# Kernel tuning notes

Measured on AMD Instinct MI355X. Metric: run time of the kernel, lower is better.

The kernel has to match this reference:

```python
import jax, jax.numpy as jnp
import numpy as np

N_NODES = 50000


def _gcn_norm(edge_index, n):
    # add self loops, compute symmetric normalization coefficients
    src = jnp.concatenate([edge_index[0], jnp.arange(n, dtype=edge_index.dtype)])
    dst = jnp.concatenate([edge_index[1], jnp.arange(n, dtype=edge_index.dtype)])
    deg = jax.ops.segment_sum(jnp.ones_like(dst, dtype=jnp.float32), dst, num_segments=n)
    dis = jnp.where(deg > 0, jax.lax.rsqrt(jnp.maximum(deg, 1.0)), 0.0)
    norm = dis[src] * dis[dst]  # [E+n]
    return src, dst, norm


def _gcn_conv(x, W, b, src, dst, norm, n):
    xw = x @ W                      # [n, out]
    msg = xw[src] * norm[:, None]   # gather + scale
    out = jax.ops.segment_sum(msg, dst, num_segments=n)
    return out + b


def setup_inputs() -> dict:
    key = jax.random.key(0)
    ks = jax.random.split(key, 12)
    n, d, h, E, P = N_NODES, 512, 512, 400000, 200000
    sc = lambda fan_in: 1.0 / np.sqrt(fan_in)
    return {
        "x": jax.random.normal(ks[0], (n, d), dtype=jnp.float32),
        "edge_index": jax.random.randint(ks[1], (2, E), 0, n, dtype=jnp.int32),
        "edge_pairs": jax.random.randint(ks[2], (2, P), 0, n, dtype=jnp.int32),
        "W1": jax.random.uniform(ks[3], (d, h), jnp.float32, -sc(d), sc(d)),
        "b1": jnp.zeros((h,), jnp.float32),
        "W2": jax.random.uniform(ks[4], (h, h), jnp.float32, -sc(h), sc(h)),
        "b2": jnp.zeros((h,), jnp.float32),
        "lpW1": jax.random.uniform(ks[5], (2 * h, h), jnp.float32, -sc(2 * h), sc(2 * h)),
        "lpb1": jax.random.uniform(ks[6], (h,), jnp.float32, -sc(2 * h), sc(2 * h)),
        "lpW2": jax.random.uniform(ks[7], (h, 1), jnp.float32, -sc(h), sc(h)),
        "lpb2": jax.random.uniform(ks[8], (1,), jnp.float32, -sc(h), sc(h)),
    }


def reference(x, edge_index, edge_pairs, W1, b1, W2, b2, lpW1, lpb1, lpW2, lpb2):
    n = x.shape[0]
    src, dst, norm = _gcn_norm(edge_index, n)
    # encoder: GCNConv -> relu -> (dropout is identity at inference) -> GCNConv
    z = _gcn_conv(x, W1, b1, src, dst, norm, n)
    z = jax.nn.relu(z)
    z = _gcn_conv(z, W2, b2, src, dst, norm, n)
    # link predictor: gather-concat MLP
    h = jnp.concatenate([z[edge_pairs[0]], z[edge_pairs[1]]], axis=-1)  # [P, 2h]
    h = jax.nn.relu(h @ lpW1 + lpb1)
    logits = (h @ lpW2 + lpb2)[:, 0]
    return jax.nn.sigmoid(logits)
```

## Files before the change

kernel.cpp:

```cpp
#include <hip/hip_runtime.h>
#include <hip/hip_bf16.h>
#include <math.h>

#define TPB 256

typedef __attribute__((ext_vector_type(8))) short bf16x8;
typedef __attribute__((ext_vector_type(4))) float f32x4;

__device__ __forceinline__ unsigned cvt_bf(float f) {
    unsigned u = __float_as_uint(f);
    u += 0x7fffu + ((u >> 16) & 1u);
    return u >> 16;
}
__device__ __forceinline__ unsigned pack2f(float a, float b) {
    __hip_bfloat162 h = __float22bfloat162_rn(float2{a, b});
    unsigned u;
    __builtin_memcpy(&u, &h, 4);
    return u;
}

__device__ __forceinline__ void gload16(const void* g, void* l) {
    __builtin_amdgcn_global_load_lds(
        (const __attribute__((address_space(1))) void*)g,
        (__attribute__((address_space(3))) void*)l, 16, 0, 0);
}


__global__ void k_hist(const int* __restrict__ dst, int* __restrict__ cnt, int E) {
    int e = blockIdx.x * TPB + threadIdx.x;
    if (e < E) atomicAdd(&cnt[dst[e]], 1);
}

__global__ __launch_bounds__(256)
void k_scan1(const int* __restrict__ cnt, int* __restrict__ incl,
             int* __restrict__ bsum, int n) {
    __shared__ int sh[256];
    const int t = threadIdx.x;
    const int i = blockIdx.x * 256 + t;
    int v = (i < n) ? cnt[i] : 0;
    sh[t] = v;
    __syncthreads();
#pragma unroll
    for (int d = 1; d < 256; d <<= 1) {
        int u = (t >= d) ? sh[t - d] : 0;
        __syncthreads();
        sh[t] += u;
        __syncthreads();
    }
    if (i < n) incl[i] = sh[t];
    if (t == 255) bsum[blockIdx.x] = sh[255];
}

__global__ __launch_bounds__(256)
void k_scan2(int* __restrict__ bsum, int* __restrict__ boff,
             int* __restrict__ row_start, int n, int nb) {
    __shared__ int sh[256];
    const int t = threadIdx.x;
    int v = (t < nb) ? bsum[t] : 0;
    sh[t] = v;
    __syncthreads();
#pragma unroll
    for (int d = 1; d < 256; d <<= 1) {
        int u = (t >= d) ? sh[t - d] : 0;
        __syncthreads();
        sh[t] += u;
        __syncthreads();
    }
    if (t < nb) boff[t] = sh[t] - v;
    if (t == nb - 1) row_start[n] = sh[t];
}

__global__ void k_scan3(const int* __restrict__ cnt, const int* __restrict__ incl,
                        const int* __restrict__ boff, int* __restrict__ row_start,
                        int* __restrict__ cursor, float* __restrict__ dis, int n) {
    int i = blockIdx.x * TPB + threadIdx.x;
    if (i >= n) return;
    int c = cnt[i];
    int ex = boff[i >> 8] + incl[i] - c;
    row_start[i] = ex;
    cursor[i] = ex;
    dis[i] = rsqrtf((float)c + 1.0f);
}

__global__ void k_fill_csr(const int* __restrict__ src, const int* __restrict__ dst,
                           const float* __restrict__ dis, int* __restrict__ cursor,
                           int* __restrict__ csr_src, float* __restrict__ csr_nrm, int E) {
    int e = blockIdx.x * TPB + threadIdx.x;
    if (e >= E) return;
    int s = src[e], d = dst[e];
    int pos = atomicAdd(&cursor[d], 1);
    csr_src[pos] = s;
    csr_nrm[pos] = dis[s] * dis[d];
}


__global__ __launch_bounds__(256)
void k_prep(const float* __restrict__ x, unsigned short* __restrict__ xbf, int n8, int nbA,
            const float* __restrict__ W1, unsigned short* __restrict__ w1t,
            const float* __restrict__ W2, unsigned short* __restrict__ w2bf,
            const float* __restrict__ lpW1, unsigned short* __restrict__ lpw1t,
            const float* __restrict__ b2, const float* __restrict__ lpb1,
            float* __restrict__ bias_big) {
    int b = blockIdx.x;
    if (b < nbA) {
        int i = b * TPB + threadIdx.x;
        if (i >= n8) return;
        float4 f0 = *(const float4*)(x + (size_t)i * 8);
        float4 f1 = *(const float4*)(x + (size_t)i * 8 + 4);
        uint4 o;
        o.x = pack2f(f0.x, f0.y); o.y = pack2f(f0.z, f0.w);
        o.z = pack2f(f1.x, f1.y); o.w = pack2f(f1.z, f1.w);
        *(uint4*)(xbf + (size_t)i * 8) = o;
        return;
    }
    b -= nbA;
    if (b < 1024) {
        int id = b * TPB + threadIdx.x;
        int nn = id >> 9, k = id & 511;
        w1t[id] = (unsigned short)cvt_bf(W1[(size_t)k * 512 + nn]);
        return;
    }
    b -= 1024;
    if (b < 128) {
        int i = b * TPB + threadIdx.x;
        float4 f0 = *(const float4*)(W2 + (size_t)i * 8);
        float4 f1 = *(const float4*)(W2 + (size_t)i * 8 + 4);
        uint4 o;
        o.x = pack2f(f0.x, f0.y); o.y = pack2f(f0.z, f0.w);
        o.z = pack2f(f1.x, f1.y); o.w = pack2f(f1.z, f1.w);
        *(uint4*)(w2bf + (size_t)i * 8) = o;
        return;
    }
    b -= 128;
    if (b < 2048) {
        int id = b * TPB + threadIdx.x;
        int j = id >> 9, k = id & 511;
        float v = (j < 512) ? lpW1[(size_t)k * 512 + j]
                            : lpW1[(size_t)(512 + k) * 512 + (j - 512)];
        lpw1t[id] = (unsigned short)cvt_bf(v);
        return;
    }
    b -= 2048;
    {
        const int j = b * 4 + (threadIdx.x >> 6);
        if (j >= 1024) return;
        const int lane = threadIdx.x & 63;
        const int col = (j < 512) ? j : (j - 512);
        const int ro = (j < 512) ? 0 : 512;
        float s = 0.f;
#pragma unroll
        for (int it = 0; it < 8; ++it) {
            int k = lane + it * 64;
            s = fmaf(b2[k], lpW1[(size_t)(ro + k) * 512 + col], s);
        }
        s += __shfl_xor(s, 1, 64);
        s += __shfl_xor(s, 2, 64);
        s += __shfl_xor(s, 4, 64);
        s += __shfl_xor(s, 8, 64);
        s += __shfl_xor(s, 16, 64);
        s += __shfl_xor(s, 32, 64);
        if (lane == 0) bias_big[j] = s + ((j < 512) ? lpb1[j] : 0.f);
    }
}


__device__ __forceinline__ void fma8(float* acc, uint4 u, float r) {
    acc[0] = fmaf(__uint_as_float(u.x << 16), r, acc[0]);
    acc[1] = fmaf(__uint_as_float(u.x & 0xffff0000u), r, acc[1]);
    acc[2] = fmaf(__uint_as_float(u.y << 16), r, acc[2]);
    acc[3] = fmaf(__uint_as_float(u.y & 0xffff0000u), r, acc[3]);
    acc[4] = fmaf(__uint_as_float(u.z << 16), r, acc[4]);
    acc[5] = fmaf(__uint_as_float(u.z & 0xffff0000u), r, acc[5]);
    acc[6] = fmaf(__uint_as_float(u.w << 16), r, acc[6]);
    acc[7] = fmaf(__uint_as_float(u.w & 0xffff0000u), r, acc[7]);
}

__global__ __launch_bounds__(256)
void k_agg_bf(const unsigned short* __restrict__ xin, const int* __restrict__ row_start,
              const int* __restrict__ csr_src, const float* __restrict__ csr_nrm,
              const float* __restrict__ dis, unsigned short* __restrict__ out, int n) {
    const int v = (blockIdx.x * TPB + threadIdx.x) >> 6;
    if (v >= n) return;
    const int lane = threadIdx.x & 63;
    const uint4* base = (const uint4*)xin;

    float d = dis[v]; float d2 = d * d;
    float acc[8];
    {
        uint4 u = base[(size_t)v * 64 + lane];
        acc[0] = d2 * __uint_as_float(u.x << 16);
        acc[1] = d2 * __uint_as_float(u.x & 0xffff0000u);
        acc[2] = d2 * __uint_as_float(u.y << 16);
        acc[3] = d2 * __uint_as_float(u.y & 0xffff0000u);
        acc[4] = d2 * __uint_as_float(u.z << 16);
        acc[5] = d2 * __uint_as_float(u.z & 0xffff0000u);
        acc[6] = d2 * __uint_as_float(u.w << 16);
        acc[7] = d2 * __uint_as_float(u.w & 0xffff0000u);
    }
    const int beg = row_start[v], end = row_start[v + 1];
    int j = beg;
    for (; j + 3 < end; j += 4) {
        int s0 = csr_src[j], s1 = csr_src[j + 1];
        int s2 = csr_src[j + 2], s3 = csr_src[j + 3];
        float r0 = csr_nrm[j], r1 = csr_nrm[j + 1];
        float r2 = csr_nrm[j + 2], r3 = csr_nrm[j + 3];
        uint4 u0 = base[(size_t)s0 * 64 + lane];
        uint4 u1 = base[(size_t)s1 * 64 + lane];
        uint4 u2 = base[(size_t)s2 * 64 + lane];
        uint4 u3 = base[(size_t)s3 * 64 + lane];
        fma8(acc, u0, r0);
        fma8(acc, u1, r1);
        fma8(acc, u2, r2);
        fma8(acc, u3, r3);
    }
    for (; j < end; ++j) {
        uint4 u = base[(size_t)csr_src[j] * 64 + lane];
        fma8(acc, u, csr_nrm[j]);
    }
    uint4 o;
    o.x = pack2f(acc[0], acc[1]); o.y = pack2f(acc[2], acc[3]);
    o.z = pack2f(acc[4], acc[5]); o.w = pack2f(acc[6], acc[7]);
    ((uint4*)out)[(size_t)v * 64 + lane] = o;
}


__global__ __launch_bounds__(256)
void k_gemm_bf(const unsigned short* __restrict__ A, const unsigned short* __restrict__ Bt,
               const float* __restrict__ bias, unsigned short* __restrict__ C,
               int M, int K, int N, int do_relu, int nbx, int m_off, int m_end) {
    const int lin = blockIdx.x;
    const int xcd = lin & 7, seq = lin >> 3;
    const int rowt = xcd + 8 * (seq / nbx);
    const int colt = seq % nbx;
    const int m0 = m_off + rowt * 128;
    if (m0 >= m_end) return;
    const int n0 = colt * 128;

    __shared__ __align__(16) char smem[16384];
    char* Asl = smem;
    char* Bsl = smem + 8192;
    const int t = threadIdx.x;
    const int wid = t >> 6, l = t & 63;
    const int wr = (wid >> 1) * 64, wc = (wid & 1) * 64;
    const int lrow = l & 15, g = l >> 4;

    const int srow = (l >> 2);
    const int cb_src = ((l & 3) * 16) ^ ((srow & 3) << 4);
    const int r0 = wid * 32 + srow, r1 = r0 + 16;
    const size_t rowA0 = (size_t)min(m0 + r0, M - 1) * K * 2;
    const size_t rowA1 = (size_t)min(m0 + r1, M - 1) * K * 2;
    const size_t rowB0 = (size_t)(n0 + r0) * K * 2;
    const size_t rowB1 = (size_t)(n0 + r1) * K * 2;
    const char* Ab = (const char*)A;
    const char* Bb = (const char*)Bt;
    char* ldsA0 = Asl + (wid * 32) * 64;
    char* ldsA1 = ldsA0 + 16 * 64;
    char* ldsB0 = Bsl + (wid * 32) * 64;
    char* ldsB1 = ldsB0 + 16 * 64;
    const int rd_off = (g * 16) ^ ((lrow & 3) << 4);

    f32x4 acc[4][4] = {};
    for (int k0 = 0; k0 < K; k0 += 32) {
        const size_t koff = (size_t)k0 * 2 + cb_src;
        gload16(Ab + rowA0 + koff, ldsA0);
        gload16(Ab + rowA1 + koff, ldsA1);
        gload16(Bb + rowB0 + koff, ldsB0);
        gload16(Bb + rowB1 + koff, ldsB1);
        __syncthreads();
        bf16x8 af[4], bfr[4];
#pragma unroll
        for (int i = 0; i < 4; ++i)
            af[i] = *(const bf16x8*)(Asl + (wr + i * 16 + lrow) * 64 + rd_off);
#pragma unroll
        for (int j = 0; j < 4; ++j)
            bfr[j] = *(const bf16x8*)(Bsl + (wc + j * 16 + lrow) * 64 + rd_off);
#pragma unroll
        for (int i = 0; i < 4; ++i)
#pragma unroll
            for (int j = 0; j < 4; ++j)
                acc[i][j] = __builtin_amdgcn_mfma_f32_16x16x32_bf16(af[i], bfr[j], acc[i][j], 0, 0, 0);
        __syncthreads();
    }

    float bv[4];
#pragma unroll
    for (int j = 0; j < 4; ++j) bv[j] = bias[n0 + wc + j * 16 + lrow];
    float* lws = (float*)(smem + wid * 4096);
    const int rrow = l >> 2, rcol = (l & 3) * 16;
#pragma unroll
    for (int i = 0; i < 4; ++i) {
#pragma unroll
        for (int e = 0; e < 4; ++e)
#pragma unroll
            for (int j = 0; j < 4; ++j) {
                float vv = acc[i][j][e] + bv[j];
                if (do_relu) vv = fmaxf(vv, 0.f);
                lws[(g * 4 + e) * 64 + j * 16 + lrow] = vv;
            }
        asm volatile("s_waitcnt lgkmcnt(0)" ::: "memory");
        __builtin_amdgcn_sched_barrier(0);
        const int grow = m0 + wr + i * 16 + rrow;
        float4 f0 = *(const float4*)&lws[rrow * 64 + rcol];
        float4 f1 = *(const float4*)&lws[rrow * 64 + rcol + 4];
        float4 f2 = *(const float4*)&lws[rrow * 64 + rcol + 8];
        float4 f3 = *(const float4*)&lws[rrow * 64 + rcol + 12];
        if (grow < M) {
            uint4 o0, o1;
            o0.x = pack2f(f0.x, f0.y); o0.y = pack2f(f0.z, f0.w);
            o0.z = pack2f(f1.x, f1.y); o0.w = pack2f(f1.z, f1.w);
            o1.x = pack2f(f2.x, f2.y); o1.y = pack2f(f2.z, f2.w);
            o1.z = pack2f(f3.x, f3.y); o1.w = pack2f(f3.z, f3.w);
            *(uint4*)(C + (size_t)grow * N + n0 + wc + rcol)     = o0;
            *(uint4*)(C + (size_t)grow * N + n0 + wc + rcol + 8) = o1;
        }
        asm volatile("s_waitcnt lgkmcnt(0)" ::: "memory");
        __builtin_amdgcn_sched_barrier(0);
    }
}


__global__ __launch_bounds__(256)
void k_pair(const unsigned short* __restrict__ uv, const int* __restrict__ pair, int P,
            const float* __restrict__ w2, const float* __restrict__ lpb2,
            float* __restrict__ out) {
    const int idx = (blockIdx.x * TPB + threadIdx.x) >> 6;
    if (idx >= P) return;
    const int lane = threadIdx.x & 63;
    const int p0n = pair[idx], p1n = pair[P + idx];
    const uint4 a = *(const uint4*)(uv + (size_t)p0n * 1024 + lane * 8);
    const uint4 b = *(const uint4*)(uv + (size_t)p1n * 1024 + 512 + lane * 8);
    const float4 w0 = *(const float4*)(w2 + lane * 8);
    const float4 w1 = *(const float4*)(w2 + lane * 8 + 4);
    const unsigned ua[4] = {a.x, a.y, a.z, a.w};
    const unsigned ub[4] = {b.x, b.y, b.z, b.w};
    const float wv[8] = {w0.x, w0.y, w0.z, w0.w, w1.x, w1.y, w1.z, w1.w};
    float s = 0.f;
#pragma unroll
    for (int q = 0; q < 4; ++q) {
        float h0 = __uint_as_float(ua[q] << 16) + __uint_as_float(ub[q] << 16);
        float h1 = __uint_as_float(ua[q] & 0xffff0000u) + __uint_as_float(ub[q] & 0xffff0000u);
        s = fmaf(fmaxf(h0, 0.f), wv[2 * q], s);
        s = fmaf(fmaxf(h1, 0.f), wv[2 * q + 1], s);
    }
    s += __shfl_xor(s, 1, 64);
    s += __shfl_xor(s, 2, 64);
    s += __shfl_xor(s, 4, 64);
    s += __shfl_xor(s, 8, 64);
    s += __shfl_xor(s, 16, 64);
    s += __shfl_xor(s, 32, 64);
    if (lane == 0) out[idx] = 1.0f / (1.0f + expf(-(s + lpb2[0])));
}


extern "C" void kernel_launch(void* const* d_in, const int* in_sizes, int n_in,
                              void* d_out, int out_size, void* d_ws, size_t ws_size,
                              hipStream_t stream) {
    const float* x    = (const float*)d_in[0];
    const int*   ei   = (const int*)d_in[1];
    const int*   ep   = (const int*)d_in[2];
    const float* W1   = (const float*)d_in[3];
    const float* b1   = (const float*)d_in[4];
    const float* W2   = (const float*)d_in[5];
    const float* b2   = (const float*)d_in[6];
    const float* lpW1 = (const float*)d_in[7];
    const float* lpb1 = (const float*)d_in[8];
    const float* lpW2 = (const float*)d_in[9];
    const float* lpb2 = (const float*)d_in[10];

    const int n = in_sizes[0] / 512;
    const int E = in_sizes[1] / 2;
    const int P = in_sizes[2] / 2;
    const int* src = ei;
    const int* dst = ei + E;

    char* w = (char*)d_ws;
    size_t off = 0;
    auto alloc = [&](size_t bytes) {
        void* p = w + off;
        off = (off + bytes + 255) & ~(size_t)255;
        return p;
    };
    int*   cnt       = (int*)alloc((size_t)n * 4);
    int*   incl      = (int*)alloc((size_t)n * 4);
    int*   bsum      = (int*)alloc((size_t)256 * 4);
    int*   boff      = (int*)alloc((size_t)256 * 4);
    int*   row_start = (int*)alloc((size_t)(n + 1) * 4);
    int*   cursor    = (int*)alloc((size_t)n * 4);
    int*   csr_src   = (int*)alloc((size_t)E * 4);
    float* csr_nrm   = (float*)alloc((size_t)E * 4);
    float* dis       = (float*)alloc((size_t)n * 4);
    unsigned short* w1t    = (unsigned short*)alloc((size_t)512 * 512 * 2);
    unsigned short* w2bf   = (unsigned short*)alloc((size_t)512 * 512 * 2);
    unsigned short* lpw1t  = (unsigned short*)alloc((size_t)1024 * 512 * 2);
    unsigned short* wfT    = (unsigned short*)alloc((size_t)1024 * 512 * 2);
    float* bias_big  = (float*)alloc((size_t)1024 * 4);
    float* zerob     = (float*)alloc((size_t)1024 * 4);
    unsigned short* bufA = (unsigned short*)alloc((size_t)n * 512 * 2);
    unsigned short* bufB = (unsigned short*)alloc((size_t)n * 512 * 2);
    unsigned short* uv   = (unsigned short*)alloc((size_t)n * 1024 * 2);

    dim3 blk(TPB);
    const int nb_n = (n + TPB - 1) / TPB;
    const int nb_E = (E + TPB - 1) / TPB;
    const int nb_scan = (n + 255) / 256;

    (void)hipMemsetAsync(cnt, 0, (size_t)n * 4, stream);
    (void)hipMemsetAsync(zerob, 0, (size_t)1024 * 4, stream);
    k_hist<<<nb_E, blk, 0, stream>>>(dst, cnt, E);
    k_scan1<<<nb_scan, 256, 0, stream>>>(cnt, incl, bsum, n);
    k_scan2<<<1, 256, 0, stream>>>(bsum, boff, row_start, n, nb_scan);
    k_scan3<<<nb_n, blk, 0, stream>>>(cnt, incl, boff, row_start, cursor, dis, n);
    k_fill_csr<<<nb_E, blk, 0, stream>>>(src, dst, dis, cursor, csr_src, csr_nrm, E);

    const int n8  = n * 64;
    const int nbA = (n8 + TPB - 1) / TPB;
    const int prep_blocks = nbA + 1024 + 128 + 2048 + 256;
    k_prep<<<prep_blocks, blk, 0, stream>>>(x, bufA, n8, nbA, W1, w1t, W2, w2bf,
                                            lpW1, lpw1t, b2, lpb1, bias_big);

    const int gy  = (n + 127) / 128;
    const int gy8 = ((gy + 7) / 8) * 8;
    const int agg_blocks = (n * 64 + TPB - 1) / TPB;

    k_gemm_bf<<<4 * 8, blk, 0, stream>>>(lpw1t, w2bf, zerob, wfT, 1024, 512, 512, 0, 4, 0, 1024);

    k_agg_bf<<<agg_blocks, blk, 0, stream>>>(bufA, row_start, csr_src, csr_nrm, dis, bufB, n);
    k_gemm_bf<<<4 * gy8, blk, 0, stream>>>(bufB, w1t, b1, bufA, n, 512, 512, 1, 4, 0, n);
    k_agg_bf<<<agg_blocks, blk, 0, stream>>>(bufA, row_start, csr_src, csr_nrm, dis, bufB, n);
    {
        const int t1 = (gy + 1) / 2;
        const int g1 = ((t1 + 7) / 8) * 8;
        const int t2 = gy - t1;
        const int g2 = ((t2 + 7) / 8) * 8;
        const int m_split = t1 * 128;
        k_gemm_bf<<<8 * g1, blk, 0, stream>>>(bufB, wfT, bias_big, uv, n, 512, 1024, 0, 8, 0, m_split);
        k_gemm_bf<<<8 * g2, blk, 0, stream>>>(bufB, wfT, bias_big, uv, n, 512, 1024, 0, 8, m_split, n);
    }

    k_pair<<<(P * 64 + TPB - 1) / TPB, blk, 0, stream>>>(uv, ep, P, lpW2, lpb2, (float*)d_out);
}
```

Before: 442.0 us.

## Software-pipeline neighbor gathers in aggregation and merge split final GEMM launch

The aggregation kernel now double-buffers its edge gathers, issuing the next four neighbor-row loads before doing the FMAs on the previous four, so more memory requests stay in flight. Separately, the final encoder-to-predictor GEMM, which was split into two launches over row ranges, becomes a single launch, and the m_off/m_end parameters are removed. The prefetching raises register pressure, and merging the launches removes whatever overlap or cache benefit the split may have offered.

```diff
diff --git a/kernel.cpp b/kernel.cpp
--- a/kernel.cpp
+++ b/kernel.cpp
@@ -199,19 +199,29 @@
     }
     const int beg = row_start[v], end = row_start[v + 1];
     int j = beg;
-    for (; j + 3 < end; j += 4) {
-        int s0 = csr_src[j], s1 = csr_src[j + 1];
-        int s2 = csr_src[j + 2], s3 = csr_src[j + 3];
-        float r0 = csr_nrm[j], r1 = csr_nrm[j + 1];
-        float r2 = csr_nrm[j + 2], r3 = csr_nrm[j + 3];
-        uint4 u0 = base[(size_t)s0 * 64 + lane];
-        uint4 u1 = base[(size_t)s1 * 64 + lane];
-        uint4 u2 = base[(size_t)s2 * 64 + lane];
-        uint4 u3 = base[(size_t)s3 * 64 + lane];
-        fma8(acc, u0, r0);
-        fma8(acc, u1, r1);
-        fma8(acc, u2, r2);
-        fma8(acc, u3, r3);
+    if (end - beg >= 4) {
+        float r[4];
+        uint4 ub[4];
+#pragma unroll
+        for (int q = 0; q < 4; ++q) r[q] = csr_nrm[j + q];
+#pragma unroll
+        for (int q = 0; q < 4; ++q) ub[q] = base[(size_t)csr_src[j + q] * 64 + lane];
+        j += 4;
+        while (j + 3 < end) {
+            float r2[4];
+            uint4 ub2[4];
+#pragma unroll
+            for (int q = 0; q < 4; ++q) r2[q] = csr_nrm[j + q];
+#pragma unroll
+            for (int q = 0; q < 4; ++q) ub2[q] = base[(size_t)csr_src[j + q] * 64 + lane];
+#pragma unroll
+            for (int q = 0; q < 4; ++q) fma8(acc, ub[q], r[q]);
+#pragma unroll
+            for (int q = 0; q < 4; ++q) { ub[q] = ub2[q]; r[q] = r2[q]; }
+            j += 4;
+        }
+#pragma unroll
+        for (int q = 0; q < 4; ++q) fma8(acc, ub[q], r[q]);
     }
     for (; j < end; ++j) {
         uint4 u = base[(size_t)csr_src[j] * 64 + lane];
@@ -227,13 +237,13 @@
 __global__ __launch_bounds__(256)
 void k_gemm_bf(const unsigned short* __restrict__ A, const unsigned short* __restrict__ Bt,
                const float* __restrict__ bias, unsigned short* __restrict__ C,
-               int M, int K, int N, int do_relu, int nbx, int m_off, int m_end) {
+               int M, int K, int N, int do_relu, int nbx) {
     const int lin = blockIdx.x;
     const int xcd = lin & 7, seq = lin >> 3;
     const int rowt = xcd + 8 * (seq / nbx);
     const int colt = seq % nbx;
-    const int m0 = m_off + rowt * 128;
-    if (m0 >= m_end) return;
+    const int m0 = rowt * 128;
+    if (m0 >= M) return;
     const int n0 = colt * 128;
 
     __shared__ __align__(16) char smem[16384];
@@ -422,20 +432,12 @@
     const int gy8 = ((gy + 7) / 8) * 8;
     const int agg_blocks = (n * 64 + TPB - 1) / TPB;
 
-    k_gemm_bf<<<4 * 8, blk, 0, stream>>>(lpw1t, w2bf, zerob, wfT, 1024, 512, 512, 0, 4, 0, 1024);
+    k_gemm_bf<<<4 * 8, blk, 0, stream>>>(lpw1t, w2bf, zerob, wfT, 1024, 512, 512, 0, 4);
 
     k_agg_bf<<<agg_blocks, blk, 0, stream>>>(bufA, row_start, csr_src, csr_nrm, dis, bufB, n);
-    k_gemm_bf<<<4 * gy8, blk, 0, stream>>>(bufB, w1t, b1, bufA, n, 512, 512, 1, 4, 0, n);
+    k_gemm_bf<<<4 * gy8, blk, 0, stream>>>(bufB, w1t, b1, bufA, n, 512, 512, 1, 4);
     k_agg_bf<<<agg_blocks, blk, 0, stream>>>(bufA, row_start, csr_src, csr_nrm, dis, bufB, n);
-    {
-        const int t1 = (gy + 1) / 2;
-        const int g1 = ((t1 + 7) / 8) * 8;
-        const int t2 = gy - t1;
-        const int g2 = ((t2 + 7) / 8) * 8;
-        const int m_split = t1 * 128;
-        k_gemm_bf<<<8 * g1, blk, 0, stream>>>(bufB, wfT, bias_big, uv, n, 512, 1024, 0, 8, 0, m_split);
-        k_gemm_bf<<<8 * g2, blk, 0, stream>>>(bufB, wfT, bias_big, uv, n, 512, 1024, 0, 8, m_split, n);
-    }
+    k_gemm_bf<<<8 * gy8, blk, 0, stream>>>(bufB, wfT, bias_big, uv, n, 512, 1024, 0, 8);
 
     k_pair<<<(P * 64 + TPB - 1) / TPB, blk, 0, stream>>>(uv, ep, P, lpW2, lpb2, (float*)d_out);
 }
```

Measured after the change: 428.7 us. 1.03x faster.
